# Kernel optimization log

Hardware: AMD Instinct MI355X
Metric: run time of the kernel (lower is better)

Reference implementation:

```python
import jax, jax.numpy as jnp
import numpy as np

N, T, P = 1024, 512, 2
H = 128  # hidden_channels == lstm_input_channels == num_fc_concat == 128


def _lin(k, out_dim, in_dim):
    # torch nn.Linear default init: U(-1/sqrt(in), 1/sqrt(in))
    b = 1.0 / np.sqrt(in_dim)
    return jax.random.uniform(k, (out_dim, in_dim), minval=-b, maxval=b, dtype=jnp.float32)


def setup_inputs() -> dict:
    key = jax.random.key(0)
    ks = jax.random.split(key, 12)
    bnd = lambda k, sh, inn: jax.random.uniform(k, sh, minval=-1.0/np.sqrt(inn), maxval=1.0/np.sqrt(inn), dtype=jnp.float32)
    return {
        "x": jax.random.normal(ks[0], (N, T, P), dtype=jnp.float32),
        "enc1_w": _lin(ks[1], 128, 2),
        "enc1_b": bnd(ks[2], (128,), 2),
        "enc2_w": _lin(ks[3], H, 128),
        "enc2_b": bnd(ks[4], (H,), 128),
        "w_ih": _lin(ks[5], 4 * H, H),   # LSTMCell weight_ih, gate order i,f,g,o; bias=False
        "w_hh": _lin(ks[6], 4 * H, H),
        "dec1_w": _lin(ks[7], H, 2 * H),
        "dec1_b": bnd(ks[8], (H,), 2 * H),
        "dec2_w": _lin(ks[9], 1, H),
        "dec2_b": bnd(ks[10], (1,), H),
    }


def reference(x, enc1_w, enc1_b, enc2_w, enc2_b, w_ih, w_hh, dec1_w, dec1_b, dec2_w, dec2_b):
    n = x.shape[0]
    # Encoder MLP applied to every (n, t) position at once: (N,T,2) -> (N,T,H)
    feat = jax.nn.relu(jnp.einsum('ntp,hp->nth', x, enc1_w) + enc1_b)
    feat = jnp.einsum('nth,oh->nto', feat, enc2_w) + enc2_b
    feat_t = jnp.swapaxes(feat, 0, 1)  # (T,N,H)

    def step(carry, xt):
        h, c = carry
        gates = xt @ w_ih.T + h @ w_hh.T  # (N, 4H)
        i, f, g, o = jnp.split(gates, 4, axis=-1)
        c = jax.nn.sigmoid(f) * c + jax.nn.sigmoid(i) * jnp.tanh(g)
        h = jax.nn.sigmoid(o) * jnp.tanh(c)
        return (h, c), h

    init = (jnp.zeros((n, H), dtype=x.dtype), jnp.zeros((n, H), dtype=x.dtype))
    # Shared LSTMCell weights run forward and backward over time
    _, h_fw = jax.lax.scan(step, init, feat_t)            # (T,N,H)
    _, h_bw_rev = jax.lax.scan(step, init, feat_t[::-1])  # (T,N,H) over reversed time
    h_bw = h_bw_rev[::-1]

    final = jax.nn.relu(jnp.concatenate([h_fw, h_bw], axis=-1))  # (T,N,2H)
    q = jax.nn.relu(jnp.einsum('tnk,hk->tnh', final, dec1_w) + dec1_b)
    q = jnp.einsum('tnh,oh->tno', q, dec2_w) + dec2_b  # (T,N,1)
    return jnp.swapaxes(q[..., 0], 0, 1)  # (N,T)
```

## Files before the change

### kernel.cpp

```cpp
#include <hip/hip_runtime.h>
#include <hip/hip_fp16.h>
#include <stdint.h>


#define TN 512
#define NB 1024

typedef __attribute__((ext_vector_type(8))) _Float16 f16x8;
typedef __attribute__((ext_vector_type(4))) float f32x4;

#define MFMA16(a,b,c) __builtin_amdgcn_mfma_f32_16x16x32_f16(a,b,c,0,0,0)
#define RCP(x) __builtin_amdgcn_rcpf(x)

__device__ __forceinline__ f16x8 cvt_frag(const float* p){
  f32x4 a = *(const f32x4*)p;
  f32x4 b = *(const f32x4*)(p+4);
  f16x8 h;
  h[0]=(_Float16)a[0]; h[1]=(_Float16)a[1]; h[2]=(_Float16)a[2]; h[3]=(_Float16)a[3];
  h[4]=(_Float16)b[0]; h[5]=(_Float16)b[1]; h[6]=(_Float16)b[2]; h[7]=(_Float16)b[3];
  return h;
}

__device__ __forceinline__ unsigned short f2h(float f){
  return __half_as_ushort(__float2half(f));
}

__global__ __launch_bounds__(256) void enc_kernel(
    const float* __restrict__ x,  const float* __restrict__ e1w,
    const float* __restrict__ e1b,const float* __restrict__ e2w,
    const float* __restrict__ e2b,
    unsigned short* __restrict__ featA, unsigned short* __restrict__ featB)
{
  __shared__ float xs[64][2];
  __shared__ unsigned int A32[64][68];
  int tid = threadIdx.x;
  long rowbase = (long)blockIdx.x * 64;
  if (tid < 128){
    int i = tid >> 1, cc = tid & 1;
    long row = rowbase + i;
    int t = (int)(row >> 10), n = (int)(row & 1023);
    xs[i][cc] = x[((size_t)n * TN + t) * 2 + cc];
  }
  int w4 = tid >> 6, lane = tid & 63, lq = lane >> 4, lr = lane & 15;
  f16x8 Bf[2][4];
  float b2v[2];
  #pragma unroll
  for (int nt2 = 0; nt2 < 2; nt2++){
    int col = (w4*2 + nt2)*16 + lr;
    b2v[nt2] = e2b[col];
    #pragma unroll
    for (int ks = 0; ks < 4; ks++)
      Bf[nt2][ks] = cvt_frag(e2w + col*128 + ks*32 + lq*8);
  }
  int q = tid >> 6, dp = tid & 63;
  float w00 = e1w[4*dp], w01 = e1w[4*dp+1], w10 = e1w[4*dp+2], w11 = e1w[4*dp+3];
  float b0 = e1b[2*dp], b1 = e1b[2*dp+1];
  __syncthreads();
  #pragma unroll
  for (int rr = 0; rr < 16; rr++){
    int r = q*16 + rr;
    float x0 = xs[r][0], x1 = xs[r][1];
    float v0 = fmaxf(w00*x0 + w01*x1 + b0, 0.f);
    float v1 = fmaxf(w10*x0 + w11*x1 + b1, 0.f);
    A32[r][dp] = (unsigned int)f2h(v0) | ((unsigned int)f2h(v1) << 16);
  }
  __syncthreads();
  #pragma unroll
  for (int Mt = 0; Mt < 4; Mt++){
    f16x8 ah[4];
    #pragma unroll
    for (int ks = 0; ks < 4; ks++)
      ah[ks] = *(const f16x8*)((const unsigned short*)&A32[Mt*16+lr][0] + ks*32 + lq*8);
    f32x4 acc0 = {0.f,0.f,0.f,0.f}, acc1 = {0.f,0.f,0.f,0.f};
    #pragma unroll
    for (int ks = 0; ks < 4; ks++){
      acc0 = MFMA16(ah[ks], Bf[0][ks], acc0);
      acc1 = MFMA16(ah[ks], Bf[1][ks], acc1);
    }
    #pragma unroll
    for (int r = 0; r < 4; r++){
      size_t row = (size_t)(rowbase + Mt*16 + lq*4 + r);
      unsigned short v0 = f2h(acc0[r] + b2v[0]);
      unsigned short v1 = f2h(acc1[r] + b2v[1]);
      featA[row*128 + (w4*2+0)*16 + lr] = v0;
      featA[row*128 + (w4*2+1)*16 + lr] = v1;
      featB[row*128 + (w4*2+0)*16 + lr] = v0;
      featB[row*128 + (w4*2+1)*16 + lr] = v1;
    }
  }
}

#define LSTM_STEP(P, PFC, PFN) do { \
    f16x8 ah[4]; \
    _Pragma("unroll") \
    for (int ks = 0; ks < 4; ks++) ah[ks] = *(const f16x8*)&hbS[P][smr][ks*32 + lq*8]; \
    _Pragma("unroll") \
    for (int ks = 0; ks < 4; ks++) PFN[ks] = *(const uint4*)(fpp + ks*32); \
    fpp += dstep; \
    f32x4 acc[4]; \
    _Pragma("unroll") \
    for (int G = 0; G < 4; G++) acc[G] = MFMA16(*(const f16x8*)&PFC[0], wg[G][0], zero4); \
    _Pragma("unroll") \
    for (int ks = 1; ks < 4; ks++){ \
      _Pragma("unroll") \
      for (int G = 0; G < 4; G++) acc[G] = MFMA16(*(const f16x8*)&PFC[ks], wg[G][ks], acc[G]); \
    } \
    _Pragma("unroll") \
    for (int ks = 0; ks < 4; ks++){ \
      _Pragma("unroll") \
      for (int G = 0; G < 4; G++) acc[G] = MFMA16(ah[ks], wg[G][4+ks], acc[G]); \
    } \
    _Pragma("unroll") \
    for (int r = 0; r < 2; r++){ \
      float iv = acc[0][r], fv = acc[1][r], gv = acc[2][r], ov = acc[3][r]; \
      float si = RCP(1.f + __expf(-iv)); \
      float sf = RCP(1.f + __expf(-fv)); \
      float so = RCP(1.f + __expf(-ov)); \
      float tg = 1.f - 2.f*RCP(__expf(2.f*gv) + 1.f); \
      c[r] = sf*c[r] + si*tg; \
      float tc = 1.f - 2.f*RCP(__expf(2.f*c[r]) + 1.f); \
      float hv = so*tc; \
      unsigned short hh = f2h(hv); \
      hbS[(P)^1][lq*2+r][w*16 + lr] = hh; \
      op[r*128] = (hv > 0.f) ? hh : (unsigned short)0; \
    } \
    op += dstep; \
    __syncthreads(); \
  } while(0)

__global__ __launch_bounds__(512, 2) void lstm_kernel(
    unsigned short* bufA, unsigned short* bufB,
    const float* __restrict__ wih, const float* __restrict__ whh)
{
  __shared__ __align__(16) unsigned short hbS[2][8][136];
  int tid = threadIdx.x, b = blockIdx.x;
  int dir = b >> 7, n0 = (b & 127) << 3;
  int w = tid >> 6, lane = tid & 63, lq = lane >> 4, lr = lane & 15;
  unsigned short* buf = dir ? bufB : bufA;

  f16x8 wg[4][8];
  #pragma unroll
  for (int G = 0; G < 4; G++){
    int gate = G*128 + w*16 + lr;
    #pragma unroll
    for (int ks = 0; ks < 8; ks++){
      const float* src = (ks < 4) ? (wih + (size_t)gate*128 + ks*32 + lq*8)
                                  : (whh + (size_t)gate*128 + (ks-4)*32 + lq*8);
      wg[G][ks] = cvt_frag(src);
    }
  }

  for (int i = tid; i < 1088; i += 512) ((unsigned int*)hbS)[i] = 0u;

  int smr = ((lr >> 2) << 1) | (lr & 1);
  float c[2] = {0.f, 0.f};
  const f32x4 zero4 = {0.f, 0.f, 0.f, 0.f};
  int t0 = dir ? (TN-1) : 0;
  long dstep = dir ? -(long)(NB*128) : (long)(NB*128);

  const unsigned short* fpp = buf + ((size_t)t0*NB + n0 + smr)*128 + lq*8;
  uint4 pfA[4], pfB[4];
  #pragma unroll
  for (int ks = 0; ks < 4; ks++) pfA[ks] = *(const uint4*)(fpp + ks*32);
  fpp += dstep;

  unsigned short* op = buf + ((size_t)t0*NB + n0 + lq*2)*128 + (w*16 + lr);
  __syncthreads();

  for (int s2 = 0; s2 < TN/2; s2++){
    LSTM_STEP(0, pfA, pfB);
    LSTM_STEP(1, pfB, pfA);
  }
}

__global__ __launch_bounds__(256) void dec_kernel(
    const unsigned short* __restrict__ hfw, const unsigned short* __restrict__ hbw,
    const float* __restrict__ d1w, const float* __restrict__ d1b,
    const float* __restrict__ d2w, const float* __restrict__ d2b,
    float* __restrict__ out)
{
  __shared__ unsigned short A[64][264];
  __shared__ float partial[4][64];
  int tid = threadIdx.x;
  long rowbase = (long)blockIdx.x * 64;
  #pragma unroll
  for (int u = 0; u < 8; u++){
    int chunk = u*256 + tid;
    int row = chunk >> 5, seg = chunk & 31;
    const unsigned short* src = (seg < 16)
        ? (hfw + ((size_t)(rowbase + row))*128 + seg*8)
        : (hbw + ((size_t)(rowbase + row))*128 + (seg-16)*8);
    *(uint4*)&A[row][seg*8] = *(const uint4*)src;
  }
  int w4 = tid >> 6, lane = tid & 63, lq = lane >> 4, lr = lane & 15;
  f16x8 Bf[2][8];
  float b1v[2], w2v[2];
  #pragma unroll
  for (int nt2 = 0; nt2 < 2; nt2++){
    int col = (w4*2 + nt2)*16 + lr;
    b1v[nt2] = d1b[col];
    w2v[nt2] = d2w[col];
    #pragma unroll
    for (int ks = 0; ks < 8; ks++)
      Bf[nt2][ks] = cvt_frag(d1w + col*256 + ks*32 + lq*8);
  }
  float b2s = d2b[0];
  __syncthreads();
  #pragma unroll
  for (int Mt = 0; Mt < 4; Mt++){
    f16x8 ah[8];
    #pragma unroll
    for (int ks = 0; ks < 8; ks++)
      ah[ks] = *(const f16x8*)&A[Mt*16+lr][ks*32 + lq*8];
    f32x4 acc0 = {0.f,0.f,0.f,0.f}, acc1 = {0.f,0.f,0.f,0.f};
    #pragma unroll
    for (int ks = 0; ks < 8; ks++){
      acc0 = MFMA16(ah[ks], Bf[0][ks], acc0);
      acc1 = MFMA16(ah[ks], Bf[1][ks], acc1);
    }
    #pragma unroll
    for (int r = 0; r < 4; r++){
      float p = fmaxf(acc0[r] + b1v[0], 0.f) * w2v[0]
              + fmaxf(acc1[r] + b1v[1], 0.f) * w2v[1];
      p += __shfl_xor(p, 1);
      p += __shfl_xor(p, 2);
      p += __shfl_xor(p, 4);
      p += __shfl_xor(p, 8);
      if (lr == 0) partial[w4][Mt*16 + lq*4 + r] = p;
    }
  }
  __syncthreads();
  if (tid < 64){
    long row = rowbase + tid;
    int t = (int)(row >> 10), n = (int)(row & 1023);
    out[(size_t)n*TN + t] = partial[0][tid] + partial[1][tid]
                          + partial[2][tid] + partial[3][tid] + b2s;
  }
}

extern "C" void kernel_launch(void* const* d_in, const int* in_sizes, int n_in,
                              void* d_out, int out_size, void* d_ws, size_t ws_size,
                              hipStream_t stream)
{
  const float* x   = (const float*)d_in[0];
  const float* e1w = (const float*)d_in[1];
  const float* e1b = (const float*)d_in[2];
  const float* e2w = (const float*)d_in[3];
  const float* e2b = (const float*)d_in[4];
  const float* wih = (const float*)d_in[5];
  const float* whh = (const float*)d_in[6];
  const float* d1w = (const float*)d_in[7];
  const float* d1b = (const float*)d_in[8];
  const float* d2w = (const float*)d_in[9];
  const float* d2b = (const float*)d_in[10];
  float* out = (float*)d_out;

  if (ws_size < ((size_t)256 << 20)) return;

  char* ws = (char*)d_ws;
  unsigned short* bufA = (unsigned short*)ws;
  unsigned short* bufB = (unsigned short*)(ws + (((size_t)128) << 20));

  hipLaunchKernelGGL(enc_kernel, dim3(8192), dim3(256), 0, stream, x, e1w, e1b, e2w, e2b, bufA, bufB);
  hipLaunchKernelGGL(lstm_kernel, dim3(256), dim3(512), 0, stream, bufA, bufB, wih, whh);
  hipLaunchKernelGGL(dec_kernel, dim3(8192), dim3(256), 0, stream, bufA, bufB, d1w, d1b, d2w, d2b, out);
}
```

Baseline: 680.0 us.

## Software-pipeline LSTM input projection of next step with current gate activations

```diff
diff --git a/kernel.cpp b/kernel.cpp
--- a/kernel.cpp
+++ b/kernel.cpp
@@ -90,40 +90,45 @@
   }
 }
 
-#define LSTM_STEP(P, PFC, PFN) do { \
-    f16x8 ah[4]; \
-    _Pragma("unroll") \
-    for (int ks = 0; ks < 4; ks++) ah[ks] = *(const f16x8*)&hbS[P][smr][ks*32 + lq*8]; \
+#define LSTM_STEP(P, ACCC, ACCN, PFC, PFN) do { \
     _Pragma("unroll") \
     for (int ks = 0; ks < 4; ks++) PFN[ks] = *(const uint4*)(fpp + ks*32); \
     fpp += dstep; \
-    f32x4 acc[4]; \
-    _Pragma("unroll") \
-    for (int G = 0; G < 4; G++) acc[G] = MFMA16(*(const f16x8*)&PFC[0], wg[G][0], zero4); \
-    _Pragma("unroll") \
-    for (int ks = 1; ks < 4; ks++){ \
+    f16x8 ah[4]; \
+    _Pragma("unroll") \
+    for (int ks = 0; ks < 4; ks++) ah[ks] = *(const f16x8*)&hbS[P][smr][ks*32 + lq*8]; \
+    _Pragma("unroll") \
+    for (int G = 0; G < 4; G++){ \
       _Pragma("unroll") \
-      for (int G = 0; G < 4; G++) acc[G] = MFMA16(*(const f16x8*)&PFC[ks], wg[G][ks], acc[G]); \
+      for (int ks = 0; ks < 4; ks++) ACCC[G] = MFMA16(ah[ks], wg[G][4+ks], ACCC[G]); \
     } \
-    _Pragma("unroll") \
-    for (int ks = 0; ks < 4; ks++){ \
-      _Pragma("unroll") \
-      for (int G = 0; G < 4; G++) acc[G] = MFMA16(ah[ks], wg[G][4+ks], acc[G]); \
-    } \
-    _Pragma("unroll") \
-    for (int r = 0; r < 2; r++){ \
-      float iv = acc[0][r], fv = acc[1][r], gv = acc[2][r], ov = acc[3][r]; \
-      float si = RCP(1.f + __expf(-iv)); \
-      float sf = RCP(1.f + __expf(-fv)); \
-      float so = RCP(1.f + __expf(-ov)); \
-      float tg = 1.f - 2.f*RCP(__expf(2.f*gv) + 1.f); \
-      c[r] = sf*c[r] + si*tg; \
-      float tc = 1.f - 2.f*RCP(__expf(2.f*c[r]) + 1.f); \
-      float hv = so*tc; \
-      unsigned short hh = f2h(hv); \
-      hbS[(P)^1][lq*2+r][w*16 + lr] = hh; \
-      op[r*128] = (hv > 0.f) ? hh : (unsigned short)0; \
-    } \
+     \
+    _Pragma("unroll") \
+    for (int G = 0; G < 4; G++) ACCN[G] = MFMA16(*(const f16x8*)&PFC[0], wg[G][0], zero4); \
+    float si0 = RCP(1.f + __expf(-ACCC[0][0])); \
+    float si1 = RCP(1.f + __expf(-ACCC[0][1])); \
+    _Pragma("unroll") \
+    for (int G = 0; G < 4; G++) ACCN[G] = MFMA16(*(const f16x8*)&PFC[1], wg[G][1], ACCN[G]); \
+    float sf0 = RCP(1.f + __expf(-ACCC[1][0])); \
+    float sf1 = RCP(1.f + __expf(-ACCC[1][1])); \
+    _Pragma("unroll") \
+    for (int G = 0; G < 4; G++) ACCN[G] = MFMA16(*(const f16x8*)&PFC[2], wg[G][2], ACCN[G]); \
+    float tg0 = 1.f - 2.f*RCP(__expf(2.f*ACCC[2][0]) + 1.f); \
+    float tg1 = 1.f - 2.f*RCP(__expf(2.f*ACCC[2][1]) + 1.f); \
+    float so0 = RCP(1.f + __expf(-ACCC[3][0])); \
+    float so1 = RCP(1.f + __expf(-ACCC[3][1])); \
+    _Pragma("unroll") \
+    for (int G = 0; G < 4; G++) ACCN[G] = MFMA16(*(const f16x8*)&PFC[3], wg[G][3], ACCN[G]); \
+    c[0] = sf0*c[0] + si0*tg0; \
+    c[1] = sf1*c[1] + si1*tg1; \
+    float tc0 = 1.f - 2.f*RCP(__expf(2.f*c[0]) + 1.f); \
+    float tc1 = 1.f - 2.f*RCP(__expf(2.f*c[1]) + 1.f); \
+    float hv0 = so0*tc0, hv1 = so1*tc1; \
+    unsigned short hh0 = f2h(hv0), hh1 = f2h(hv1); \
+    hbS[(P)^1][lq*2+0][w*16 + lr] = hh0; \
+    hbS[(P)^1][lq*2+1][w*16 + lr] = hh1; \
+    op[0]   = (hv0 > 0.f) ? hh0 : (unsigned short)0; \
+    op[128] = (hv1 > 0.f) ? hh1 : (unsigned short)0; \
     op += dstep; \
     __syncthreads(); \
   } while(0)
@@ -161,15 +166,27 @@
   const unsigned short* fpp = buf + ((size_t)t0*NB + n0 + smr)*128 + lq*8;
   uint4 pfA[4], pfB[4];
   #pragma unroll
+  for (int ks = 0; ks < 4; ks++) pfB[ks] = *(const uint4*)(fpp + ks*32);
+  fpp += dstep;
+  #pragma unroll
   for (int ks = 0; ks < 4; ks++) pfA[ks] = *(const uint4*)(fpp + ks*32);
   fpp += dstep;
 
+  f32x4 accA[4], accB[4];
+  #pragma unroll
+  for (int G = 0; G < 4; G++) accA[G] = MFMA16(*(const f16x8*)&pfB[0], wg[G][0], zero4);
+  #pragma unroll
+  for (int ks = 1; ks < 4; ks++){
+    #pragma unroll
+    for (int G = 0; G < 4; G++) accA[G] = MFMA16(*(const f16x8*)&pfB[ks], wg[G][ks], accA[G]);
+  }
+
   unsigned short* op = buf + ((size_t)t0*NB + n0 + lq*2)*128 + (w*16 + lr);
   __syncthreads();
 
   for (int s2 = 0; s2 < TN/2; s2++){
-    LSTM_STEP(0, pfA, pfB);
-    LSTM_STEP(1, pfB, pfA);
+    LSTM_STEP(0, accA, accB, pfA, pfB);
+    LSTM_STEP(1, accB, accA, pfB, pfA);
   }
 }
 
```

After: 677.0 us. About the same (-0.4%).

## Split LSTM block into producer waves for input projection and consumer waves for recurrence

Applied to the files above, without the earlier changes.

```diff
diff --git a/kernel.cpp b/kernel.cpp
--- a/kernel.cpp
+++ b/kernel.cpp
@@ -90,86 +90,140 @@
   }
 }
 
-#define LSTM_STEP(P, PFC, PFN) do { \
-    f16x8 ah[4]; \
-    _Pragma("unroll") \
-    for (int ks = 0; ks < 4; ks++) ah[ks] = *(const f16x8*)&hbS[P][smr][ks*32 + lq*8]; \
-    _Pragma("unroll") \
-    for (int ks = 0; ks < 4; ks++) PFN[ks] = *(const uint4*)(fpp + ks*32); \
-    fpp += dstep; \
-    f32x4 acc[4]; \
-    _Pragma("unroll") \
-    for (int G = 0; G < 4; G++) acc[G] = MFMA16(*(const f16x8*)&PFC[0], wg[G][0], zero4); \
-    _Pragma("unroll") \
-    for (int ks = 1; ks < 4; ks++){ \
-      _Pragma("unroll") \
-      for (int G = 0; G < 4; G++) acc[G] = MFMA16(*(const f16x8*)&PFC[ks], wg[G][ks], acc[G]); \
-    } \
-    _Pragma("unroll") \
-    for (int ks = 0; ks < 4; ks++){ \
-      _Pragma("unroll") \
-      for (int G = 0; G < 4; G++) acc[G] = MFMA16(ah[ks], wg[G][4+ks], acc[G]); \
-    } \
-    _Pragma("unroll") \
-    for (int r = 0; r < 2; r++){ \
-      float iv = acc[0][r], fv = acc[1][r], gv = acc[2][r], ov = acc[3][r]; \
-      float si = RCP(1.f + __expf(-iv)); \
-      float sf = RCP(1.f + __expf(-fv)); \
-      float so = RCP(1.f + __expf(-ov)); \
-      float tg = 1.f - 2.f*RCP(__expf(2.f*gv) + 1.f); \
-      c[r] = sf*c[r] + si*tg; \
-      float tc = 1.f - 2.f*RCP(__expf(2.f*c[r]) + 1.f); \
-      float hv = so*tc; \
-      unsigned short hh = f2h(hv); \
-      hbS[(P)^1][lq*2+r][w*16 + lr] = hh; \
-      op[r*128] = (hv > 0.f) ? hh : (unsigned short)0; \
-    } \
-    op += dstep; \
-    __syncthreads(); \
-  } while(0)
-
 __global__ __launch_bounds__(512, 2) void lstm_kernel(
     unsigned short* bufA, unsigned short* bufB,
     const float* __restrict__ wih, const float* __restrict__ whh)
 {
-  __shared__ __align__(16) unsigned short hbS[2][8][136];
+  __shared__ __align__(16) float slotf[2][2][6144];
+  __shared__ __align__(16) unsigned short hbS[2][16][136];
   int tid = threadIdx.x, b = blockIdx.x;
   int dir = b >> 7, n0 = (b & 127) << 3;
   int w = tid >> 6, lane = tid & 63, lq = lane >> 4, lr = lane & 15;
   unsigned short* buf = dir ? bufB : bufA;
-
-  f16x8 wg[4][8];
-  #pragma unroll
-  for (int G = 0; G < 4; G++){
-    int gate = G*128 + w*16 + lr;
-    #pragma unroll
-    for (int ks = 0; ks < 8; ks++){
-      const float* src = (ks < 4) ? (wih + (size_t)gate*128 + ks*32 + lq*8)
-                                  : (whh + (size_t)gate*128 + (ks-4)*32 + lq*8);
-      wg[G][ks] = cvt_frag(src);
-    }
-  }
-
-  for (int i = tid; i < 1088; i += 512) ((unsigned int*)hbS)[i] = 0u;
-
-  int smr = ((lr >> 2) << 1) | (lr & 1);
-  float c[2] = {0.f, 0.f};
+  long dstep = dir ? -(long)(NB*128) : (long)(NB*128);
+  long t0 = dir ? (TN-1) : 0;
   const f32x4 zero4 = {0.f, 0.f, 0.f, 0.f};
-  int t0 = dir ? (TN-1) : 0;
-  long dstep = dir ? -(long)(NB*128) : (long)(NB*128);
-
-  const unsigned short* fpp = buf + ((size_t)t0*NB + n0 + smr)*128 + lq*8;
-  uint4 pfA[4], pfB[4];
-  #pragma unroll
-  for (int ks = 0; ks < 4; ks++) pfA[ks] = *(const uint4*)(fpp + ks*32);
-  fpp += dstep;
-
-  unsigned short* op = buf + ((size_t)t0*NB + n0 + lq*2)*128 + (w*16 + lr);
-  __syncthreads();
-
-  for (int s2 = 0; s2 < TN/2; s2++){
-    LSTM_STEP(0, pfA, pfB);
-    LSTM_STEP(1, pfB, pfA);
+
+  for (int i = tid; i < 2176; i += 512) ((unsigned int*)hbS)[i] = 0u;
+
+  if (w >= 4){
+    int pw = w - 4;
+    f16x8 bw[8][4];
+    #pragma unroll
+    for (int j = 0; j < 8; j++){
+      #pragma unroll
+      for (int ks = 0; ks < 4; ks++)
+        bw[j][ks] = cvt_frag(wih + (size_t)(pw*128 + j*16 + lr)*128 + ks*32 + lq*8);
+    }
+    const unsigned short* fpp = buf + ((size_t)t0*NB + n0 + (lr & 7))*128
+                              + (long)(lr >> 3)*dstep + lq*8;
+    __syncthreads();
+    {
+      uint4 pa[4];
+      #pragma unroll
+      for (int ks = 0; ks < 4; ks++) pa[ks] = *(const uint4*)(fpp + ks*32);
+      fpp += 2*dstep;
+      float* sb = &slotf[0][lq >> 1][0] + (lq & 1)*4;
+      #pragma unroll
+      for (int j = 0; j < 8; j++){
+        f32x4 a = MFMA16(*(const f16x8*)&pa[0], bw[j][0], zero4);
+        #pragma unroll
+        for (int ks = 1; ks < 4; ks++) a = MFMA16(*(const f16x8*)&pa[ks], bw[j][ks], a);
+        *(f32x4*)(sb + (size_t)(pw*128 + j*16 + lr)*12) = a;
+      }
+    }
+    __syncthreads();
+    for (int p = 0; p < 256; p++){
+      float* sb = &slotf[(p & 1) ^ 1][lq >> 1][0] + (lq & 1)*4;
+      uint4 pa[4];
+      #pragma unroll
+      for (int ks = 0; ks < 4; ks++) pa[ks] = *(const uint4*)(fpp + ks*32);
+      fpp += 2*dstep;
+      #pragma unroll
+      for (int j = 0; j < 4; j++){
+        f32x4 a = MFMA16(*(const f16x8*)&pa[0], bw[j][0], zero4);
+        #pragma unroll
+        for (int ks = 1; ks < 4; ks++) a = MFMA16(*(const f16x8*)&pa[ks], bw[j][ks], a);
+        *(f32x4*)(sb + (size_t)(pw*128 + j*16 + lr)*12) = a;
+      }
+      __syncthreads();
+      #pragma unroll
+      for (int j = 4; j < 8; j++){
+        f32x4 a = MFMA16(*(const f16x8*)&pa[0], bw[j][0], zero4);
+        #pragma unroll
+        for (int ks = 1; ks < 4; ks++) a = MFMA16(*(const f16x8*)&pa[ks], bw[j][ks], a);
+        *(f32x4*)(sb + (size_t)(pw*128 + j*16 + lr)*12) = a;
+      }
+      __syncthreads();
+    }
+  } else {
+    int cw = w;
+    f16x8 bh[4][2][4];
+    #pragma unroll
+    for (int G = 0; G < 4; G++){
+      #pragma unroll
+      for (int dt = 0; dt < 2; dt++){
+        #pragma unroll
+        for (int ks = 0; ks < 4; ks++)
+          bh[G][dt][ks] = cvt_frag(whh + (size_t)(G*128 + cw*32 + dt*16 + lr)*128 + ks*32 + lq*8);
+      }
+    }
+    int chb = ((lane >> 4) & 1) * 4;
+    int dim = 32*cw + (lane >> 5)*16 + lr;
+    unsigned short* op = buf + ((size_t)t0*NB + n0 + chb)*128 + dim;
+    float c4[4] = {0.f, 0.f, 0.f, 0.f};
+
+#define CONSUME(SP) do { \
+      f16x8 ah[4]; \
+      _Pragma("unroll") \
+      for (int ks = 0; ks < 4; ks++) ah[ks] = *(const f16x8*)&hbS[SP][lr][ks*32 + lq*8]; \
+      const float* sb = &slotf[p & 1][SP][0] + (lq & 1)*4; \
+      f32x4 acc[4][2]; \
+      _Pragma("unroll") \
+      for (int G = 0; G < 4; G++){ \
+        _Pragma("unroll") \
+        for (int dt = 0; dt < 2; dt++){ \
+          acc[G][dt] = *(const f32x4*)(sb + (size_t)(G*128 + cw*32 + dt*16 + lr)*12); \
+          _Pragma("unroll") \
+          for (int ks = 0; ks < 4; ks++) \
+            acc[G][dt] = MFMA16(ah[ks], bh[G][dt][ks], acc[G][dt]); \
+        } \
+      } \
+      f32x4 av[4]; \
+      _Pragma("unroll") \
+      for (int G = 0; G < 4; G++){ \
+        _Pragma("unroll") \
+        for (int r = 0; r < 4; r++){ \
+          float sw = __shfl_xor(acc[G][1][r], 32); \
+          av[G][r] = (lane < 32) ? acc[G][0][r] : sw; \
+        } \
+      } \
+      _Pragma("unroll") \
+      for (int r = 0; r < 4; r++){ \
+        float iv = av[0][r], fv = av[1][r], gv = av[2][r], ov = av[3][r]; \
+        float si = RCP(1.f + __expf(-iv)); \
+        float sf = RCP(1.f + __expf(-fv)); \
+        float so = RCP(1.f + __expf(-ov)); \
+        float tg = 1.f - 2.f*RCP(__expf(2.f*gv) + 1.f); \
+        c4[r] = sf*c4[r] + si*tg; \
+        float tc = 1.f - 2.f*RCP(__expf(2.f*c4[r]) + 1.f); \
+        float hv = so*tc; \
+        unsigned short hh = f2h(hv); \
+        hbS[(SP)^1][chb + r][dim] = hh; \
+        op[r*128] = (hv > 0.f) ? hh : (unsigned short)0; \
+      } \
+      op += dstep; \
+    } while(0)
+
+    __syncthreads();
+    __syncthreads();
+    for (int p = 0; p < 256; p++){
+      CONSUME(0);
+      __syncthreads();
+      CONSUME(1);
+      __syncthreads();
+    }
+#undef CONSUME
   }
 }
 
```

Result: slower. 746.5 us (+9.8%).
